# Optimization experiments

Measured on AMD Instinct MI355X. Metric: run time of the kernel, lower is better.

The kernel has to match this reference:

```python
import jax, jax.numpy as jnp
import numpy as np

C = 1024
FACTOR = 4
C_INT = C * FACTOR


def setup_inputs() -> dict:
    key = jax.random.key(0)
    ks = jax.random.split(key, 6)
    act = jax.random.normal(ks[0], (4, 2048, C), dtype=jnp.float32)
    mask = jnp.ones((4, 2048), dtype=jnp.float32)
    # LayerNorm params
    ln_scale = jnp.ones((C,), dtype=jnp.float32)
    ln_bias = jnp.zeros((C,), dtype=jnp.float32)
    # Linear 1 (init='linear'): lecun-normal-ish
    w1 = jax.random.normal(ks[1], (C, C_INT), dtype=jnp.float32) / np.sqrt(C)
    b1 = jnp.zeros((C_INT,), dtype=jnp.float32)
    # Linear 2 (init='final' -> zeros in AF2; use small random so grads are nontrivial)
    w2 = jax.random.normal(ks[2], (C_INT, C), dtype=jnp.float32) * 0.02
    b2 = jnp.zeros((C,), dtype=jnp.float32)
    return {"act": act, "mask": mask, "ln_scale": ln_scale, "ln_bias": ln_bias,
            "w1": w1, "b1": b1, "w2": w2, "b2": b2}


def _layernorm(x, scale, bias, eps=1e-5):
    mu = jnp.mean(x, axis=-1, keepdims=True)
    var = jnp.mean(jnp.square(x - mu), axis=-1, keepdims=True)
    return (x - mu) * jax.lax.rsqrt(var + eps) * scale + bias


def reference(act, mask, ln_scale, ln_bias, w1, b1, w2, b2):
    # mask is accepted but unused, matching the original forward.
    x = _layernorm(act, ln_scale, ln_bias)
    h = jax.nn.relu(jnp.einsum('bsc,cf->bsf', x, w1) + b1)
    return jnp.einsum('bsf,fc->bsc', h, w2) + b2
```

## Files before the change

### kernel.cpp

```cpp
#include <hip/hip_runtime.h>
#include <hip/hip_bf16.h>
#include <cstdint>

typedef unsigned short u16;
typedef __bf16 bf16x8 __attribute__((ext_vector_type(8)));
typedef float floatx4 __attribute__((ext_vector_type(4)));

#define AS1 __attribute__((address_space(1)))
#define AS3 __attribute__((address_space(3)))

#define SCHED0  __builtin_amdgcn_sched_barrier(0)
#define BARRIER __builtin_amdgcn_s_barrier()

static __device__ __forceinline__ u16 f2bf(float f) {
    union { float f; unsigned int u; } v; v.f = f;
    unsigned int u = v.u;
    return (u16)((u + 0x7FFFu + ((u >> 16) & 1u)) >> 16);
}

static __device__ __forceinline__ unsigned lds_off(const u16* p) {
    return (unsigned)(unsigned long long)(const AS3 u16*)p;
}
static __device__ __forceinline__ bf16x8 ds_read8(unsigned off) {
    bf16x8 r;
    asm volatile("ds_read_b128 %0, %1" : "=v"(r) : "v"(off));
    return r;
}

__device__ __forceinline__ void transpose_body(
    const float* __restrict__ in, u16* __restrict__ out,
    int R, int Ccols, int bx, int by, int tid, float (*tile)[33])
{
    const int r0 = by * 128, c0 = bx * 32;
#pragma unroll
    for (int p = 0; p < 4; ++p) {
        const int f = p * 256 + tid;
        const int r = f >> 3, c4 = (f & 7) * 4;
        const float4 v = *(const float4*)&in[(size_t)(r0 + r) * Ccols + c0 + c4];
        tile[r][c4 + 0] = v.x; tile[r][c4 + 1] = v.y;
        tile[r][c4 + 2] = v.z; tile[r][c4 + 3] = v.w;
    }
    __syncthreads();
    const int wv = tid >> 6, ln = tid & 63;
#pragma unroll
    for (int i = 0; i < 8; ++i) {
        const int c = i * 4 + wv;
        ushort2 o = { f2bf(tile[ln * 2][c]), f2bf(tile[ln * 2 + 1][c]) };
        *(ushort2*)&out[(size_t)(c0 + c) * R + r0 + ln * 2] = o;
    }
}

__global__ __launch_bounds__(256)
void prep(const float* __restrict__ w1, const float* __restrict__ w2,
          const float* __restrict__ act, const float* __restrict__ ln_scale,
          const float* __restrict__ ln_bias,
          u16* __restrict__ W1t, u16* __restrict__ W2t, u16* __restrict__ X)
{
    __shared__ float tile[128][33];
    const int id  = blockIdx.x;
    const int tid = threadIdx.x;

    if (id < 1024) {
        transpose_body(w1, W1t, 1024, 4096, id & 127, id >> 7, tid, tile);
        return;
    }
    if (id < 2048) {
        const int t = id - 1024;
        transpose_body(w2, W2t, 4096, 1024, t & 31, t >> 5, tid, tile);
        return;
    }
    const int row = id - 2048;
    const float4 v = ((const float4*)(act + (size_t)row * 1024))[tid];
    float s  = v.x + v.y + v.z + v.w;
    float ss = v.x * v.x + v.y * v.y + v.z * v.z + v.w * v.w;
#pragma unroll
    for (int off = 32; off > 0; off >>= 1) {
        s  += __shfl_xor(s, off, 64);
        ss += __shfl_xor(ss, off, 64);
    }
    float* red = &tile[0][0];
    const int wave = tid >> 6, lane = tid & 63;
    if (lane == 0) { red[wave] = s; red[4 + wave] = ss; }
    __syncthreads();
    s  = red[0] + red[1] + red[2] + red[3];
    ss = red[4] + red[5] + red[6] + red[7];
    const float mu  = s * (1.0f / 1024.0f);
    const float var = ss * (1.0f / 1024.0f) - mu * mu;
    const float rs  = rsqrtf(var + 1e-5f);
    const float4 sc = ((const float4*)ln_scale)[tid];
    const float4 bi = ((const float4*)ln_bias)[tid];
    ushort4 o;
    o.x = f2bf((v.x - mu) * rs * sc.x + bi.x);
    o.y = f2bf((v.y - mu) * rs * sc.y + bi.y);
    o.z = f2bf((v.z - mu) * rs * sc.z + bi.z);
    o.w = f2bf((v.w - mu) * rs * sc.w + bi.w);
    ((ushort4*)(X + (size_t)row * 1024))[tid] = o;
}

__global__ __launch_bounds__(512, 2)
void gemm1(const u16* __restrict__ A, const u16* __restrict__ Bt,
           const float* __restrict__ bias, u16* __restrict__ H)
{
    constexpr int K = 1024, N = 4096;
    constexpr int ASZ = 256 * 64;
    __shared__ __align__(16) u16 Alds[2 * ASZ];
    __shared__ __align__(16) u16 Blds[2 * ASZ];

    const int tid  = threadIdx.x;
    const int wave = tid >> 6;
    const int lane = tid & 63;
    const int srow = lane >> 3;
    const int sst  = lane & 7;
    const int quad = lane >> 4;
    const int l16  = lane & 15;
    const int rkey = l16 & 7;
    const int wm   = wave >> 2;
    const int wn   = wave & 3;

    const int id = blockIdx.x;
    const int bm = id & 31;
    const int bn = id >> 5;

    const u16* Ag = A  + (size_t)bm * 256 * K;
    const u16* Bg = Bt + (size_t)bn * 256 * K;

    auto stA = [&](int buf, int c, int k0) {
        const int row = c * 64 + wave * 8 + srow;
        const int col = (sst ^ (row & 7)) * 8;
        __builtin_amdgcn_global_load_lds(
            (AS1 void*)(Ag + (size_t)row * K + k0 + col),
            (AS3 void*)(&Alds[buf * ASZ + c * 4096 + wave * 512]), 16, 0, 0);
    };
    auto stB = [&](int buf, int c, int k0) {
        const int row = c * 64 + wave * 8 + srow;
        const int col = (sst ^ (row & 7)) * 8;
        __builtin_amdgcn_global_load_lds(
            (AS1 void*)(Bg + (size_t)row * K + k0 + col),
            (AS3 void*)(&Blds[buf * ASZ + c * 4096 + wave * 512]), 16, 0, 0);
    };

    const unsigned Ab = lds_off(&Alds[0]);
    const unsigned Bb = lds_off(&Blds[0]);
    unsigned aoff[8][2], boff[4][2];
#pragma unroll
    for (int mi = 0; mi < 8; ++mi)
#pragma unroll
        for (int kh = 0; kh < 2; ++kh)
            aoff[mi][kh] = ((wm * 128 + mi * 16 + l16) * 64 +
                            ((kh * 4 + quad) ^ rkey) * 8) * 2;
#pragma unroll
    for (int ni = 0; ni < 4; ++ni)
#pragma unroll
        for (int kh = 0; kh < 2; ++kh)
            boff[ni][kh] = ((wn * 64 + ni * 16 + l16) * 64 +
                            ((kh * 4 + quad) ^ rkey) * 8) * 2;

    floatx4 acc[8][4];
#pragma unroll
    for (int i = 0; i < 8; ++i)
#pragma unroll
        for (int j = 0; j < 4; ++j)
            acc[i][j] = (floatx4){0.f, 0.f, 0.f, 0.f};

    constexpr int NT = K / 64;

    stA(0, 0, 0); stA(0, 2, 0);
    stB(0, 0, 0); stB(0, 1, 0); stB(0, 2, 0); stB(0, 3, 0);
    stA(0, 1, 0); stA(0, 3, 0);
    asm volatile("s_waitcnt vmcnt(2)" ::: "memory");
    SCHED0; BARRIER; SCHED0;

    bf16x8 bres[4][2];
    bf16x8 afr[2][2][2];
    for (int t = 0; t < NT; ++t) {
        const unsigned ab = Ab + (unsigned)((t & 1) * ASZ * 2);
        const unsigned bb = Bb + (unsigned)((t & 1) * ASZ * 2);
        const int nb = (t + 1) & 1;
        const int k1 = (t + 1) * 64;
        const bool st = (t + 1 < NT);

#pragma unroll
        for (int p = 0; p < 4; ++p) {
            if (p == 0) {
#pragma unroll
                for (int ni = 0; ni < 4; ++ni)
#pragma unroll
                    for (int kh = 0; kh < 2; ++kh)
                        bres[ni][kh] = ds_read8(bb + boff[ni][kh]);
#pragma unroll
                for (int sl = 0; sl < 2; ++sl)
#pragma unroll
                    for (int j = 0; j < 2; ++j)
#pragma unroll
                        for (int kh = 0; kh < 2; ++kh)
                            afr[sl][j][kh] = ds_read8(ab + aoff[sl * 2 + j][kh]);
            } else if (p < 3) {
#pragma unroll
                for (int j = 0; j < 2; ++j)
#pragma unroll
                    for (int kh = 0; kh < 2; ++kh)
                        afr[(p + 1) & 1][j][kh] =
                            ds_read8(ab + aoff[(p + 1) * 2 + j][kh]);
            }
            if (st) {
                if (p == 0)      { stA(nb, 0, k1); stA(nb, 2, k1); }
                else if (p == 1) { stB(nb, 0, k1); stB(nb, 1, k1); }
                else if (p == 2) { stB(nb, 2, k1); stB(nb, 3, k1); }
                else             { stA(nb, 1, k1); stA(nb, 3, k1); }
            }
            if (p == 3) asm volatile("s_waitcnt lgkmcnt(0)" ::: "memory");
            else        asm volatile("s_waitcnt lgkmcnt(4)" ::: "memory");
            SCHED0;
            __builtin_amdgcn_s_setprio(1);
#pragma unroll
            for (int kh = 0; kh < 2; ++kh)
#pragma unroll
                for (int j = 0; j < 2; ++j)
#pragma unroll
                    for (int ni = 0; ni < 4; ++ni)
                        acc[2 * p + j][ni] = __builtin_amdgcn_mfma_f32_16x16x32_bf16(
                            bres[ni][kh], afr[p & 1][j][kh], acc[2 * p + j][ni], 0, 0, 0);
            __builtin_amdgcn_s_setprio(0);
            SCHED0;
            if (p == 0) {
                if (st) asm volatile("s_waitcnt vmcnt(2)" ::: "memory");
                else    asm volatile("s_waitcnt vmcnt(0)" ::: "memory");
            }
            if (p == 3 && st)
                asm volatile("s_waitcnt vmcnt(2)" ::: "memory");
            BARRIER; SCHED0;
        }
    }

    const int mbase = bm * 256 + wm * 128;
    const int nbase = bn * 256 + wn * 64;
#pragma unroll
    for (int mi = 0; mi < 8; ++mi) {
        const int m = mbase + mi * 16 + l16;
#pragma unroll
        for (int ni = 0; ni < 4; ++ni) {
            const int n0 = nbase + ni * 16 + quad * 4;
            const float4 bv = *(const float4*)&bias[n0];
            float v0 = fmaxf(acc[mi][ni][0] + bv.x, 0.f);
            float v1 = fmaxf(acc[mi][ni][1] + bv.y, 0.f);
            float v2 = fmaxf(acc[mi][ni][2] + bv.z, 0.f);
            float v3 = fmaxf(acc[mi][ni][3] + bv.w, 0.f);
            ushort4 o = { f2bf(v0), f2bf(v1), f2bf(v2), f2bf(v3) };
            *(ushort4*)&H[(size_t)m * N + n0] = o;
        }
    }
}

__global__ __launch_bounds__(512, 2)
void gemm2(const u16* __restrict__ A, const u16* __restrict__ Bt,
           const float* __restrict__ bias, float* __restrict__ Cout)
{
    constexpr int K = 4096, N = 1024;
    constexpr int ASZ = 2 * 256 * 32;
    constexpr int BSZ = 2 * 128 * 32;
    __shared__ __align__(16) u16 Alds[3 * ASZ];
    __shared__ __align__(16) u16 Blds[3 * BSZ];

    const int tid  = threadIdx.x;
    const int wave = tid >> 6;
    const int lane = tid & 63;
    const int quad = lane >> 4;
    const int l16  = lane & 15;
    const int key4 = (l16 >> 1) & 3;
    const int wm   = wave >> 1;
    const int wn   = wave & 1;

    const int id = blockIdx.x;
    const int bm = id & 31;
    const int bn = id >> 5;

    const u16* Ag = A  + (size_t)bm * 256 * K;
    const u16* Bg = Bt + (size_t)bn * 128 * K;

    auto stA = [&](int buf, int kh, int c, int k0) {
        const int row = c * 128 + wave * 16 + (lane >> 2);
        const int col = kh * 32 + ((lane & 3) ^ ((row >> 1) & 3)) * 8;
        __builtin_amdgcn_global_load_lds(
            (AS1 void*)(Ag + (size_t)row * K + k0 + col),
            (AS3 void*)(&Alds[buf * ASZ + kh * 8192 + c * 4096 + wave * 512]),
            16, 0, 0);
    };
    auto stB = [&](int buf, int kh, int k0) {
        const int row = wave * 16 + (lane >> 2);
        const int col = kh * 32 + ((lane & 3) ^ ((row >> 1) & 3)) * 8;
        __builtin_amdgcn_global_load_lds(
            (AS1 void*)(Bg + (size_t)row * K + k0 + col),
            (AS3 void*)(&Blds[buf * BSZ + kh * 4096 + wave * 512]), 16, 0, 0);
    };

    const unsigned Ab = lds_off(&Alds[0]);
    const unsigned Bb = lds_off(&Blds[0]);
    unsigned aoff[4], boff[4];
#pragma unroll
    for (int mi = 0; mi < 4; ++mi)
        aoff[mi] = ((wm * 64 + mi * 16 + l16) * 32 + (quad ^ key4) * 8) * 2;
#pragma unroll
    for (int ni = 0; ni < 4; ++ni)
        boff[ni] = ((wn * 64 + ni * 16 + l16) * 32 + (quad ^ key4) * 8) * 2;

    floatx4 acc[4][4];
#pragma unroll
    for (int i = 0; i < 4; ++i)
#pragma unroll
        for (int j = 0; j < 4; ++j)
            acc[i][j] = (floatx4){0.f, 0.f, 0.f, 0.f};

    constexpr int NT = K / 64;

    stA(0, 0, 0, 0);  stA(0, 0, 1, 0);  stB(0, 0, 0);
    stA(0, 1, 0, 0);  stA(0, 1, 1, 0);  stB(0, 1, 0);
    stA(1, 0, 0, 64); stA(1, 0, 1, 64); stB(1, 0, 64);
    stA(1, 1, 0, 64); stA(1, 1, 1, 64); stB(1, 1, 64);
    asm volatile("s_waitcnt vmcnt(6)" ::: "memory");
    SCHED0; BARRIER; SCHED0;

    bf16x8 fa[2][4], fb[2][4];
#pragma unroll
    for (int i = 0; i < 4; ++i) {
        fa[0][i] = ds_read8(Ab + aoff[i]);
        fb[0][i] = ds_read8(Bb + boff[i]);
    }

    int bs0 = 0, bs1 = 1, bs2 = 2;
    for (int t = 0; t < NT; ++t) {
        const int k2 = (t + 2) * 64;
        const bool st  = (t + 2 < NT);
        const bool rd1 = (t + 1 < NT);
        const unsigned a0 = Ab + (unsigned)(bs0 * ASZ * 2);
        const unsigned b0 = Bb + (unsigned)(bs0 * BSZ * 2);
        const unsigned a1 = Ab + (unsigned)(bs1 * ASZ * 2);
        const unsigned b1 = Bb + (unsigned)(bs1 * BSZ * 2);

#pragma unroll
        for (int i = 0; i < 4; ++i) {
            fa[1][i] = ds_read8(a0 + 16384u + aoff[i]);
            fb[1][i] = ds_read8(b0 + 8192u  + boff[i]);
        }
        if (st) { stA(bs2, 0, 0, k2); stA(bs2, 0, 1, k2); stB(bs2, 0, k2); }
        asm volatile("s_waitcnt lgkmcnt(8)" ::: "memory");
        SCHED0;
        __builtin_amdgcn_s_setprio(1);
#pragma unroll
        for (int mi = 0; mi < 4; ++mi)
#pragma unroll
            for (int ni = 0; ni < 4; ++ni)
                acc[mi][ni] = __builtin_amdgcn_mfma_f32_16x16x32_bf16(
                    fb[0][ni], fa[0][mi], acc[mi][ni], 0, 0, 0);
        __builtin_amdgcn_s_setprio(0);
        SCHED0;
        if (st)       asm volatile("s_waitcnt vmcnt(6)" ::: "memory");
        else if (rd1) asm volatile("s_waitcnt vmcnt(3)" ::: "memory");
        BARRIER; SCHED0;

        if (rd1) {
#pragma unroll
            for (int i = 0; i < 4; ++i) {
                fa[0][i] = ds_read8(a1 + aoff[i]);
                fb[0][i] = ds_read8(b1 + boff[i]);
            }
        }
        if (st) { stA(bs2, 1, 0, k2); stA(bs2, 1, 1, k2); stB(bs2, 1, k2); }
        if (rd1) asm volatile("s_waitcnt lgkmcnt(8)" ::: "memory");
        else     asm volatile("s_waitcnt lgkmcnt(0)" ::: "memory");
        SCHED0;
        __builtin_amdgcn_s_setprio(1);
#pragma unroll
        for (int mi = 0; mi < 4; ++mi)
#pragma unroll
            for (int ni = 0; ni < 4; ++ni)
                acc[mi][ni] = __builtin_amdgcn_mfma_f32_16x16x32_bf16(
                    fb[1][ni], fa[1][mi], acc[mi][ni], 0, 0, 0);
        __builtin_amdgcn_s_setprio(0);
        SCHED0;
        if (st)       asm volatile("s_waitcnt vmcnt(6)" ::: "memory");
        else if (rd1) asm volatile("s_waitcnt vmcnt(0)" ::: "memory");
        BARRIER; SCHED0;

        const int tmp = bs0; bs0 = bs1; bs1 = bs2; bs2 = tmp;
    }

    const int mbase = bm * 256 + wm * 64;
    const int nbase = bn * 128 + wn * 64;
#pragma unroll
    for (int mi = 0; mi < 4; ++mi) {
        const int m = mbase + mi * 16 + l16;
#pragma unroll
        for (int ni = 0; ni < 4; ++ni) {
            const int n0 = nbase + ni * 16 + quad * 4;
            const float4 bv = *(const float4*)&bias[n0];
            float4 o = { acc[mi][ni][0] + bv.x, acc[mi][ni][1] + bv.y,
                         acc[mi][ni][2] + bv.z, acc[mi][ni][3] + bv.w };
            *(float4*)&Cout[(size_t)m * N + n0] = o;
        }
    }
}

extern "C" void kernel_launch(void* const* d_in, const int* in_sizes, int n_in,
                              void* d_out, int out_size, void* d_ws, size_t ws_size,
                              hipStream_t stream)
{
    const float* act      = (const float*)d_in[0];
    const float* ln_scale = (const float*)d_in[2];
    const float* ln_bias  = (const float*)d_in[3];
    const float* w1       = (const float*)d_in[4];
    const float* b1       = (const float*)d_in[5];
    const float* w2       = (const float*)d_in[6];
    const float* b2       = (const float*)d_in[7];
    float* out = (float*)d_out;

    const int M = 8192, C = 1024, CI = 4096;

    u16* X   = (u16*)d_ws;
    u16* W1t = X   + (size_t)M * C;
    u16* W2t = W1t + (size_t)CI * C;
    u16* H   = W2t + (size_t)C * CI;

    prep<<<10240, 256, 0, stream>>>(w1, w2, act, ln_scale, ln_bias, W1t, W2t, X);
    gemm1<<<(M / 256) * (CI / 256), 512, 0, stream>>>(X, W1t, b1, H);
    gemm2<<<(M / 256) * (C / 128), 512, 0, stream>>>(H, W2t, b2, out);
}
```

Before: 249.0 us.

## Restructure GEMM1 main loop into k-half phases with cross-tile fragment prefetch

Rewrites the first GEMM's inner loop so each phase covers four M-fragments at one k-half. The LDS fragments for the next tile are now prefetched during the last phase of the current tile, and fewer fragment registers are live at once. Global-to-LDS loads are regrouped so all A chunks issue in phase 0 and all B chunks in phase 1, with a full vmcnt(0) wait before the last phase. It also marks the ds_read output as early-clobber and wraps the waitcnt instructions in template helpers. The risk is that waiting for all global loads to finish exposes memory latency, and the prologue now waits for the full first tile before starting.

```diff
diff --git a/kernel.cpp b/kernel.cpp
--- a/kernel.cpp
+++ b/kernel.cpp
@@ -23,8 +23,19 @@
 }
 static __device__ __forceinline__ bf16x8 ds_read8(unsigned off) {
     bf16x8 r;
-    asm volatile("ds_read_b128 %0, %1" : "=v"(r) : "v"(off));
+    asm volatile("ds_read_b128 %0, %1" : "=&v"(r) : "v"(off));
     return r;
+}
+
+template <int N> __device__ __forceinline__ void wvm() {
+    if constexpr (N == 0) asm volatile("s_waitcnt vmcnt(0)" ::: "memory");
+    else if constexpr (N == 3) asm volatile("s_waitcnt vmcnt(3)" ::: "memory");
+    else if constexpr (N == 6) asm volatile("s_waitcnt vmcnt(6)" ::: "memory");
+}
+template <int N> __device__ __forceinline__ void wlg() {
+    if constexpr (N == 0) asm volatile("s_waitcnt lgkmcnt(0)" ::: "memory");
+    else if constexpr (N == 4) asm volatile("s_waitcnt lgkmcnt(4)" ::: "memory");
+    else if constexpr (N == 8) asm volatile("s_waitcnt lgkmcnt(8)" ::: "memory");
 }
 
 __device__ __forceinline__ void transpose_body(
@@ -139,8 +150,8 @@
             (AS3 void*)(&Blds[buf * ASZ + c * 4096 + wave * 512]), 16, 0, 0);
     };
 
-    const unsigned Ab = lds_off(&Alds[0]);
-    const unsigned Bb = lds_off(&Blds[0]);
+    const unsigned Abase = lds_off(&Alds[0]);
+    const unsigned Bbase = lds_off(&Blds[0]);
     unsigned aoff[8][2], boff[4][2];
 #pragma unroll
     for (int mi = 0; mi < 8; ++mi)
@@ -164,72 +175,91 @@
 
     constexpr int NT = K / 64;
 
-    stA(0, 0, 0); stA(0, 2, 0);
+    stA(0, 0, 0); stA(0, 2, 0); stA(0, 1, 0); stA(0, 3, 0);
     stB(0, 0, 0); stB(0, 1, 0); stB(0, 2, 0); stB(0, 3, 0);
-    stA(0, 1, 0); stA(0, 3, 0);
-    asm volatile("s_waitcnt vmcnt(2)" ::: "memory");
+    wvm<0>();
     SCHED0; BARRIER; SCHED0;
 
-    bf16x8 bres[4][2];
-    bf16x8 afr[2][2][2];
+    bf16x8 afrX[4], afrY[4], bres0[4], bres1[4];
+#pragma unroll
+    for (int j = 0; j < 4; ++j) afrX[j] = ds_read8(Abase + aoff[j][0]);
+#pragma unroll
+    for (int ni = 0; ni < 4; ++ni) bres0[ni] = ds_read8(Bbase + boff[ni][0]);
+
     for (int t = 0; t < NT; ++t) {
-        const unsigned ab = Ab + (unsigned)((t & 1) * ASZ * 2);
-        const unsigned bb = Bb + (unsigned)((t & 1) * ASZ * 2);
-        const int nb = (t + 1) & 1;
+        const int cur = t & 1, nb = cur ^ 1;
+        const unsigned ab0 = Abase + (unsigned)(cur * ASZ * 2);
+        const unsigned bb0 = Bbase + (unsigned)(cur * ASZ * 2);
+        const unsigned abn = Abase + (unsigned)(nb * ASZ * 2);
+        const unsigned bbn = Bbase + (unsigned)(nb * ASZ * 2);
         const int k1 = (t + 1) * 64;
         const bool st = (t + 1 < NT);
 
 #pragma unroll
-        for (int p = 0; p < 4; ++p) {
-            if (p == 0) {
-#pragma unroll
-                for (int ni = 0; ni < 4; ++ni)
-#pragma unroll
-                    for (int kh = 0; kh < 2; ++kh)
-                        bres[ni][kh] = ds_read8(bb + boff[ni][kh]);
-#pragma unroll
-                for (int sl = 0; sl < 2; ++sl)
-#pragma unroll
-                    for (int j = 0; j < 2; ++j)
-#pragma unroll
-                        for (int kh = 0; kh < 2; ++kh)
-                            afr[sl][j][kh] = ds_read8(ab + aoff[sl * 2 + j][kh]);
-            } else if (p < 3) {
-#pragma unroll
-                for (int j = 0; j < 2; ++j)
-#pragma unroll
-                    for (int kh = 0; kh < 2; ++kh)
-                        afr[(p + 1) & 1][j][kh] =
-                            ds_read8(ab + aoff[(p + 1) * 2 + j][kh]);
-            }
-            if (st) {
-                if (p == 0)      { stA(nb, 0, k1); stA(nb, 2, k1); }
-                else if (p == 1) { stB(nb, 0, k1); stB(nb, 1, k1); }
-                else if (p == 2) { stB(nb, 2, k1); stB(nb, 3, k1); }
-                else             { stA(nb, 1, k1); stA(nb, 3, k1); }
-            }
-            if (p == 3) asm volatile("s_waitcnt lgkmcnt(0)" ::: "memory");
-            else        asm volatile("s_waitcnt lgkmcnt(4)" ::: "memory");
-            SCHED0;
-            __builtin_amdgcn_s_setprio(1);
-#pragma unroll
-            for (int kh = 0; kh < 2; ++kh)
-#pragma unroll
-                for (int j = 0; j < 2; ++j)
-#pragma unroll
-                    for (int ni = 0; ni < 4; ++ni)
-                        acc[2 * p + j][ni] = __builtin_amdgcn_mfma_f32_16x16x32_bf16(
-                            bres[ni][kh], afr[p & 1][j][kh], acc[2 * p + j][ni], 0, 0, 0);
-            __builtin_amdgcn_s_setprio(0);
-            SCHED0;
-            if (p == 0) {
-                if (st) asm volatile("s_waitcnt vmcnt(2)" ::: "memory");
-                else    asm volatile("s_waitcnt vmcnt(0)" ::: "memory");
-            }
-            if (p == 3 && st)
-                asm volatile("s_waitcnt vmcnt(2)" ::: "memory");
-            BARRIER; SCHED0;
-        }
+        for (int j = 0; j < 4; ++j) afrY[j] = ds_read8(ab0 + aoff[4 + j][0]);
+#pragma unroll
+        for (int ni = 0; ni < 4; ++ni) bres1[ni] = ds_read8(bb0 + boff[ni][1]);
+        if (st) { stA(nb, 0, k1); stA(nb, 2, k1); stA(nb, 1, k1); stA(nb, 3, k1); }
+        wlg<8>();
+        SCHED0;
+        __builtin_amdgcn_s_setprio(1);
+#pragma unroll
+        for (int j = 0; j < 4; ++j)
+#pragma unroll
+            for (int ni = 0; ni < 4; ++ni)
+                acc[j][ni] = __builtin_amdgcn_mfma_f32_16x16x32_bf16(
+                    bres0[ni], afrX[j], acc[j][ni], 0, 0, 0);
+        __builtin_amdgcn_s_setprio(0);
+        SCHED0; BARRIER; SCHED0;
+
+#pragma unroll
+        for (int j = 0; j < 4; ++j) afrX[j] = ds_read8(ab0 + aoff[j][1]);
+        if (st) { stB(nb, 0, k1); stB(nb, 1, k1); stB(nb, 2, k1); stB(nb, 3, k1); }
+        wlg<8>();
+        SCHED0;
+        __builtin_amdgcn_s_setprio(1);
+#pragma unroll
+        for (int j = 0; j < 4; ++j)
+#pragma unroll
+            for (int ni = 0; ni < 4; ++ni)
+                acc[4 + j][ni] = __builtin_amdgcn_mfma_f32_16x16x32_bf16(
+                    bres0[ni], afrY[j], acc[4 + j][ni], 0, 0, 0);
+        __builtin_amdgcn_s_setprio(0);
+        SCHED0; BARRIER; SCHED0;
+
+#pragma unroll
+        for (int j = 0; j < 4; ++j) afrY[j] = ds_read8(ab0 + aoff[4 + j][1]);
+        wlg<4>();
+        SCHED0;
+        __builtin_amdgcn_s_setprio(1);
+#pragma unroll
+        for (int j = 0; j < 4; ++j)
+#pragma unroll
+            for (int ni = 0; ni < 4; ++ni)
+                acc[j][ni] = __builtin_amdgcn_mfma_f32_16x16x32_bf16(
+                    bres1[ni], afrX[j], acc[j][ni], 0, 0, 0);
+        __builtin_amdgcn_s_setprio(0);
+        SCHED0;
+        if (st) wvm<0>();
+        BARRIER; SCHED0;
+
+        if (st) {
+#pragma unroll
+            for (int j = 0; j < 4; ++j) afrX[j] = ds_read8(abn + aoff[j][0]);
+#pragma unroll
+            for (int ni = 0; ni < 4; ++ni) bres0[ni] = ds_read8(bbn + boff[ni][0]);
+            wlg<8>();
+        } else wlg<0>();
+        SCHED0;
+        __builtin_amdgcn_s_setprio(1);
+#pragma unroll
+        for (int j = 0; j < 4; ++j)
+#pragma unroll
+            for (int ni = 0; ni < 4; ++ni)
+                acc[4 + j][ni] = __builtin_amdgcn_mfma_f32_16x16x32_bf16(
+                    bres1[ni], afrY[j], acc[4 + j][ni], 0, 0, 0);
+        __builtin_amdgcn_s_setprio(0);
+        SCHED0; BARRIER; SCHED0;
     }
 
     const int mbase = bm * 256 + wm * 128;
@@ -316,7 +346,7 @@
     stA(0, 1, 0, 0);  stA(0, 1, 1, 0);  stB(0, 1, 0);
     stA(1, 0, 0, 64); stA(1, 0, 1, 64); stB(1, 0, 64);
     stA(1, 1, 0, 64); stA(1, 1, 1, 64); stB(1, 1, 64);
-    asm volatile("s_waitcnt vmcnt(6)" ::: "memory");
+    wvm<6>();
     SCHED0; BARRIER; SCHED0;
 
     bf16x8 fa[2][4], fb[2][4];
@@ -342,7 +372,7 @@
             fb[1][i] = ds_read8(b0 + 8192u  + boff[i]);
         }
         if (st) { stA(bs2, 0, 0, k2); stA(bs2, 0, 1, k2); stB(bs2, 0, k2); }
-        asm volatile("s_waitcnt lgkmcnt(8)" ::: "memory");
+        wlg<8>();
         SCHED0;
         __builtin_amdgcn_s_setprio(1);
 #pragma unroll
@@ -353,8 +383,8 @@
                     fb[0][ni], fa[0][mi], acc[mi][ni], 0, 0, 0);
         __builtin_amdgcn_s_setprio(0);
         SCHED0;
-        if (st)       asm volatile("s_waitcnt vmcnt(6)" ::: "memory");
-        else if (rd1) asm volatile("s_waitcnt vmcnt(3)" ::: "memory");
+        if (st)       wvm<6>();
+        else if (rd1) wvm<3>();
         BARRIER; SCHED0;
 
         if (rd1) {
@@ -365,8 +395,7 @@
             }
         }
         if (st) { stA(bs2, 1, 0, k2); stA(bs2, 1, 1, k2); stB(bs2, 1, k2); }
-        if (rd1) asm volatile("s_waitcnt lgkmcnt(8)" ::: "memory");
-        else     asm volatile("s_waitcnt lgkmcnt(0)" ::: "memory");
+        if (rd1) wlg<8>(); else wlg<0>();
         SCHED0;
         __builtin_amdgcn_s_setprio(1);
 #pragma unroll
@@ -377,8 +406,8 @@
                     fb[1][ni], fa[1][mi], acc[mi][ni], 0, 0, 0);
         __builtin_amdgcn_s_setprio(0);
         SCHED0;
-        if (st)       asm volatile("s_waitcnt vmcnt(6)" ::: "memory");
-        else if (rd1) asm volatile("s_waitcnt vmcnt(0)" ::: "memory");
+        if (st)       wvm<6>();
+        else if (rd1) wvm<0>();
         BARRIER; SCHED0;
 
         const int tmp = bs0; bs0 = bs1; bs1 = bs2; bs2 = tmp;
```

Measured after the change: 248.8 us. Within noise of the previous version (-0.1%).

## Remap GEMM block indices for XCD L2 locality and widen weight transpose tiles

Applied to the files above, without the earlier changes.

gemm1 now remaps block IDs so that each XCD (blockIdx & 7) gets a fixed pair of N-column tiles, which keeps the W1 tile hot in that XCD's L2. gemm2 switches to N-fastest ordering so consecutive blocks share the same H rows. The prep transpose handles 128x64 tiles instead of 128x32, halving the number of transpose blocks. The ds_read output constraint becomes early-clobber and the waitcnt asm is wrapped in templates, both cosmetic or correctness-hardening; the gains depend on how the hardware dispatches blocks across XCDs.

```diff
diff --git a/kernel.cpp b/kernel.cpp
--- a/kernel.cpp
+++ b/kernel.cpp
@@ -23,19 +23,31 @@
 }
 static __device__ __forceinline__ bf16x8 ds_read8(unsigned off) {
     bf16x8 r;
-    asm volatile("ds_read_b128 %0, %1" : "=v"(r) : "v"(off));
+    asm volatile("ds_read_b128 %0, %1" : "=&v"(r) : "v"(off));
     return r;
+}
+
+template <int N> __device__ __forceinline__ void wvm() {
+    if constexpr (N == 0) asm volatile("s_waitcnt vmcnt(0)" ::: "memory");
+    else if constexpr (N == 2) asm volatile("s_waitcnt vmcnt(2)" ::: "memory");
+    else if constexpr (N == 3) asm volatile("s_waitcnt vmcnt(3)" ::: "memory");
+    else if constexpr (N == 6) asm volatile("s_waitcnt vmcnt(6)" ::: "memory");
+}
+template <int N> __device__ __forceinline__ void wlg() {
+    if constexpr (N == 0) asm volatile("s_waitcnt lgkmcnt(0)" ::: "memory");
+    else if constexpr (N == 4) asm volatile("s_waitcnt lgkmcnt(4)" ::: "memory");
+    else if constexpr (N == 8) asm volatile("s_waitcnt lgkmcnt(8)" ::: "memory");
 }
 
 __device__ __forceinline__ void transpose_body(
     const float* __restrict__ in, u16* __restrict__ out,
-    int R, int Ccols, int bx, int by, int tid, float (*tile)[33])
+    int R, int Ccols, int bx, int by, int tid, float (*tile)[65])
 {
-    const int r0 = by * 128, c0 = bx * 32;
-#pragma unroll
-    for (int p = 0; p < 4; ++p) {
+    const int r0 = by * 128, c0 = bx * 64;
+#pragma unroll
+    for (int p = 0; p < 8; ++p) {
         const int f = p * 256 + tid;
-        const int r = f >> 3, c4 = (f & 7) * 4;
+        const int r = f >> 4, c4 = (f & 15) * 4;
         const float4 v = *(const float4*)&in[(size_t)(r0 + r) * Ccols + c0 + c4];
         tile[r][c4 + 0] = v.x; tile[r][c4 + 1] = v.y;
         tile[r][c4 + 2] = v.z; tile[r][c4 + 3] = v.w;
@@ -43,7 +55,7 @@
     __syncthreads();
     const int wv = tid >> 6, ln = tid & 63;
 #pragma unroll
-    for (int i = 0; i < 8; ++i) {
+    for (int i = 0; i < 16; ++i) {
         const int c = i * 4 + wv;
         ushort2 o = { f2bf(tile[ln * 2][c]), f2bf(tile[ln * 2 + 1][c]) };
         *(ushort2*)&out[(size_t)(c0 + c) * R + r0 + ln * 2] = o;
@@ -56,20 +68,20 @@
           const float* __restrict__ ln_bias,
           u16* __restrict__ W1t, u16* __restrict__ W2t, u16* __restrict__ X)
 {
-    __shared__ float tile[128][33];
+    __shared__ float tile[128][65];
     const int id  = blockIdx.x;
     const int tid = threadIdx.x;
 
+    if (id < 512) {
+        transpose_body(w1, W1t, 1024, 4096, id & 63, id >> 6, tid, tile);
+        return;
+    }
     if (id < 1024) {
-        transpose_body(w1, W1t, 1024, 4096, id & 127, id >> 7, tid, tile);
+        const int t = id - 512;
+        transpose_body(w2, W2t, 4096, 1024, t & 15, t >> 4, tid, tile);
         return;
     }
-    if (id < 2048) {
-        const int t = id - 1024;
-        transpose_body(w2, W2t, 4096, 1024, t & 31, t >> 5, tid, tile);
-        return;
-    }
-    const int row = id - 2048;
+    const int row = id - 1024;
     const float4 v = ((const float4*)(act + (size_t)row * 1024))[tid];
     float s  = v.x + v.y + v.z + v.w;
     float ss = v.x * v.x + v.y * v.y + v.z * v.z + v.w * v.w;
@@ -117,9 +129,11 @@
     const int wm   = wave >> 2;
     const int wn   = wave & 3;
 
-    const int id = blockIdx.x;
-    const int bm = id & 31;
-    const int bn = id >> 5;
+    const int orig = blockIdx.x;
+    const int xcd  = orig & 7;
+    const int j    = orig >> 3;
+    const int bm   = j & 31;
+    const int bn   = 2 * xcd + (j >> 5);
 
     const u16* Ag = A  + (size_t)bm * 256 * K;
     const u16* Bg = Bt + (size_t)bn * 256 * K;
@@ -159,15 +173,15 @@
 #pragma unroll
     for (int i = 0; i < 8; ++i)
 #pragma unroll
-        for (int j = 0; j < 4; ++j)
-            acc[i][j] = (floatx4){0.f, 0.f, 0.f, 0.f};
+        for (int jj = 0; jj < 4; ++jj)
+            acc[i][jj] = (floatx4){0.f, 0.f, 0.f, 0.f};
 
     constexpr int NT = K / 64;
 
     stA(0, 0, 0); stA(0, 2, 0);
     stB(0, 0, 0); stB(0, 1, 0); stB(0, 2, 0); stB(0, 3, 0);
     stA(0, 1, 0); stA(0, 3, 0);
-    asm volatile("s_waitcnt vmcnt(2)" ::: "memory");
+    wvm<2>();
     SCHED0; BARRIER; SCHED0;
 
     bf16x8 bres[4][2];
@@ -190,17 +204,17 @@
 #pragma unroll
                 for (int sl = 0; sl < 2; ++sl)
 #pragma unroll
-                    for (int j = 0; j < 2; ++j)
+                    for (int jj = 0; jj < 2; ++jj)
 #pragma unroll
                         for (int kh = 0; kh < 2; ++kh)
-                            afr[sl][j][kh] = ds_read8(ab + aoff[sl * 2 + j][kh]);
+                            afr[sl][jj][kh] = ds_read8(ab + aoff[sl * 2 + jj][kh]);
             } else if (p < 3) {
 #pragma unroll
-                for (int j = 0; j < 2; ++j)
+                for (int jj = 0; jj < 2; ++jj)
 #pragma unroll
                     for (int kh = 0; kh < 2; ++kh)
-                        afr[(p + 1) & 1][j][kh] =
-                            ds_read8(ab + aoff[(p + 1) * 2 + j][kh]);
+                        afr[(p + 1) & 1][jj][kh] =
+                            ds_read8(ab + aoff[(p + 1) * 2 + jj][kh]);
             }
             if (st) {
                 if (p == 0)      { stA(nb, 0, k1); stA(nb, 2, k1); }
@@ -208,26 +222,23 @@
                 else if (p == 2) { stB(nb, 2, k1); stB(nb, 3, k1); }
                 else             { stA(nb, 1, k1); stA(nb, 3, k1); }
             }
-            if (p == 3) asm volatile("s_waitcnt lgkmcnt(0)" ::: "memory");
-            else        asm volatile("s_waitcnt lgkmcnt(4)" ::: "memory");
+            if (p == 3) wlg<0>(); else wlg<4>();
             SCHED0;
             __builtin_amdgcn_s_setprio(1);
 #pragma unroll
             for (int kh = 0; kh < 2; ++kh)
 #pragma unroll
-                for (int j = 0; j < 2; ++j)
+                for (int jj = 0; jj < 2; ++jj)
 #pragma unroll
                     for (int ni = 0; ni < 4; ++ni)
-                        acc[2 * p + j][ni] = __builtin_amdgcn_mfma_f32_16x16x32_bf16(
-                            bres[ni][kh], afr[p & 1][j][kh], acc[2 * p + j][ni], 0, 0, 0);
+                        acc[2 * p + jj][ni] = __builtin_amdgcn_mfma_f32_16x16x32_bf16(
+                            bres[ni][kh], afr[p & 1][jj][kh], acc[2 * p + jj][ni], 0, 0, 0);
             __builtin_amdgcn_s_setprio(0);
             SCHED0;
             if (p == 0) {
-                if (st) asm volatile("s_waitcnt vmcnt(2)" ::: "memory");
-                else    asm volatile("s_waitcnt vmcnt(0)" ::: "memory");
+                if (st) wvm<2>(); else wvm<0>();
             }
-            if (p == 3 && st)
-                asm volatile("s_waitcnt vmcnt(2)" ::: "memory");
+            if (p == 3 && st) wvm<2>();
             BARRIER; SCHED0;
         }
     }
@@ -270,9 +281,9 @@
     const int wm   = wave >> 1;
     const int wn   = wave & 1;
 
-    const int id = blockIdx.x;
-    const int bm = id & 31;
-    const int bn = id >> 5;
+    const int orig = blockIdx.x;
+    const int bn   = orig & 7;
+    const int bm   = orig >> 3;
 
     const u16* Ag = A  + (size_t)bm * 256 * K;
     const u16* Bg = Bt + (size_t)bn * 128 * K;
@@ -316,7 +327,7 @@
     stA(0, 1, 0, 0);  stA(0, 1, 1, 0);  stB(0, 1, 0);
     stA(1, 0, 0, 64); stA(1, 0, 1, 64); stB(1, 0, 64);
     stA(1, 1, 0, 64); stA(1, 1, 1, 64); stB(1, 1, 64);
-    asm volatile("s_waitcnt vmcnt(6)" ::: "memory");
+    wvm<6>();
     SCHED0; BARRIER; SCHED0;
 
     bf16x8 fa[2][4], fb[2][4];
@@ -342,7 +353,7 @@
             fb[1][i] = ds_read8(b0 + 8192u  + boff[i]);
         }
         if (st) { stA(bs2, 0, 0, k2); stA(bs2, 0, 1, k2); stB(bs2, 0, k2); }
-        asm volatile("s_waitcnt lgkmcnt(8)" ::: "memory");
+        wlg<8>();
         SCHED0;
         __builtin_amdgcn_s_setprio(1);
 #pragma unroll
@@ -353,8 +364,8 @@
                     fb[0][ni], fa[0][mi], acc[mi][ni], 0, 0, 0);
         __builtin_amdgcn_s_setprio(0);
         SCHED0;
-        if (st)       asm volatile("s_waitcnt vmcnt(6)" ::: "memory");
-        else if (rd1) asm volatile("s_waitcnt vmcnt(3)" ::: "memory");
+        if (st)       wvm<6>();
+        else if (rd1) wvm<3>();
         BARRIER; SCHED0;
 
         if (rd1) {
@@ -365,8 +376,7 @@
             }
         }
         if (st) { stA(bs2, 1, 0, k2); stA(bs2, 1, 1, k2); stB(bs2, 1, k2); }
-        if (rd1) asm volatile("s_waitcnt lgkmcnt(8)" ::: "memory");
-        else     asm volatile("s_waitcnt lgkmcnt(0)" ::: "memory");
+        if (rd1) wlg<8>(); else wlg<0>();
         SCHED0;
         __builtin_amdgcn_s_setprio(1);
 #pragma unroll
@@ -377,8 +387,8 @@
                     fb[1][ni], fa[1][mi], acc[mi][ni], 0, 0, 0);
         __builtin_amdgcn_s_setprio(0);
         SCHED0;
-        if (st)       asm volatile("s_waitcnt vmcnt(6)" ::: "memory");
-        else if (rd1) asm volatile("s_waitcnt vmcnt(0)" ::: "memory");
+        if (st)       wvm<6>();
+        else if (rd1) wvm<0>();
         BARRIER; SCHED0;
 
         const int tmp = bs0; bs0 = bs1; bs1 = bs2; bs2 = tmp;
@@ -420,7 +430,7 @@
     u16* W2t = W1t + (size_t)CI * C;
     u16* H   = W2t + (size_t)C * CI;
 
-    prep<<<10240, 256, 0, stream>>>(w1, w2, act, ln_scale, ln_bias, W1t, W2t, X);
+    prep<<<9216, 256, 0, stream>>>(w1, w2, act, ln_scale, ln_bias, W1t, W2t, X);
     gemm1<<<(M / 256) * (CI / 256), 512, 0, stream>>>(X, W1t, b1, H);
     gemm2<<<(M / 256) * (C / 128), 512, 0, stream>>>(H, W2t, b2, out);
 }
```

Result: slower. 274.2 us (+10.2%).
